# Performance work log

Measured on AMD Instinct MI355X. Metric: run time of the kernel, lower is better.

Reference implementation:

```python
import jax, jax.numpy as jnp
import numpy as np

NY, NU, NH = 8, 8, 256
T, NB = 2048, 64


def setup_inputs() -> dict:
    key = jax.random.key(0)
    ks = jax.random.split(key, 10)
    return {
        "_y0": jax.random.normal(ks[0], (NB, NY), dtype=jnp.float32),
        "_U": jax.random.normal(ks[1], (T, NB, NU), dtype=jnp.float32),
        "lmbd_cont_real": jax.random.uniform(ks[2], (NH // 2,), dtype=jnp.float32),
        "lmbd_cont_imag": jax.random.uniform(ks[3], (NH // 2,), dtype=jnp.float32),
        "B": jax.random.normal(ks[4], (NH, NU), dtype=jnp.float32) / np.sqrt(NU).astype(np.float32),
        "multiplier_on_B": jnp.zeros((NH,), dtype=jnp.float32),
        "W_y2x": jax.random.normal(ks[5], (NH, NY), dtype=jnp.float32) / np.sqrt(NY).astype(np.float32),
        "b_y2x": jax.random.normal(ks[6], (NH,), dtype=jnp.float32) * 0.01,
        "W_x2y": jax.random.normal(ks[7], (NY, NH), dtype=jnp.float32) / np.sqrt(NH).astype(np.float32),
        "b_x2y": jax.random.normal(ks[8], (NY,), dtype=jnp.float32) * 0.01,
    }


def reference(_y0, _U, lmbd_cont_real, lmbd_cont_imag, B, multiplier_on_B,
              W_y2x, b_y2x, W_x2y, b_x2y):
    H2 = lmbd_cont_real.shape[0]
    # input drive: (T, NB, NH)
    Bu = jnp.einsum('tbu,hu->tbh', _U, B) * jnp.exp(multiplier_on_B)
    # stable complex-conjugate-pair eigenvalues
    r = jnp.exp(-jnp.abs(lmbd_cont_real))
    theta = (jnp.pi / 2) * lmbd_cont_imag
    re = r * jnp.cos(theta)
    im = r * jnp.sin(theta)
    # initial state from y0
    x0 = _y0 @ W_y2x.T + b_y2x  # (NB, NH)

    def step(x, bu):
        x1, x2 = x[:, :H2], x[:, H2:]
        # A = [[diag(re), -diag(im)], [diag(im), diag(re)]]; x <- x A^T + bu
        nx = jnp.concatenate([re * x1 - im * x2, im * x1 + re * x2], axis=1) + bu
        return nx, nx

    _, X = jax.lax.scan(step, x0, Bu)  # X: (T, NB, NH)
    Y = X @ W_x2y.T + b_x2y  # (T, NB, NY)
    return Y
```

## Files before the change

kernel.cpp:

```cpp
#include <hip/hip_runtime.h>
#include <math.h>

#define T_   2048
#define NB_  64
#define NU_  8
#define NY_  8
#define NH_  256
#define H2_  128
#define CCH  64
#define LCH  32
#define TT_  2

#define BUF_FLOATS (CCH*NB_*H2_*2)
static const float PI_HALF = 1.5707963267948966f;


__global__ __launch_bounds__(64) void k_local(
    const float* __restrict__ U, const float* __restrict__ lr,
    const float* __restrict__ li, const float* __restrict__ B,
    const float* __restrict__ mult, float* __restrict__ c_buf)
{
    const int k = blockIdx.x >> 6;
    const int b = blockIdx.x & 63;
    const int j = threadIdx.x;

    float r1  = expf(-fabsf(lr[j]));
    float t1  = PI_HALF * li[j];
    float re1 = r1 * cosf(t1), im1 = r1 * sinf(t1);
    float r2  = expf(-fabsf(lr[j+64]));
    float t2  = PI_HALF * li[j+64];
    float re2 = r2 * cosf(t2), im2 = r2 * sinf(t2);

    float B1[NU_], B2[NU_], B3[NU_], B4[NU_];
    {
        float s1 = expf(mult[j]),      s2 = expf(mult[j+128]);
        float s3 = expf(mult[j+64]),   s4 = expf(mult[j+192]);
        #pragma unroll
        for (int i = 0; i < NU_; i++) {
            B1[i] = B[(j      )*NU_ + i] * s1;
            B2[i] = B[(j + 128)*NU_ + i] * s2;
            B3[i] = B[(j +  64)*NU_ + i] * s3;
            B4[i] = B[(j + 192)*NU_ + i] * s4;
        }
    }

    __shared__ float uS[LCH*NU_];
    {
        int t = j >> 1, half = j & 1;
        float4 v = *(const float4*)(U + ((size_t)(k*LCH + t)*NB_ + b)*NU_ + half*4);
        ((float4*)uS)[j] = v;
    }
    __syncthreads();

    float x1a=0.f, x2a=0.f, x1b=0.f, x2b=0.f;
    #pragma unroll 8
    for (int t = 0; t < LCH; t++) {
        float4 u0 = ((const float4*)uS)[2*t+0];
        float4 u1 = ((const float4*)uS)[2*t+1];
        float u[NU_] = {u0.x,u0.y,u0.z,u0.w,u1.x,u1.y,u1.z,u1.w};
        float bu1=0.f, bu2=0.f, bu3=0.f, bu4=0.f;
        #pragma unroll
        for (int i = 0; i < NU_; i++) {
            bu1 = fmaf(u[i], B1[i], bu1);
            bu2 = fmaf(u[i], B2[i], bu2);
            bu3 = fmaf(u[i], B3[i], bu3);
            bu4 = fmaf(u[i], B4[i], bu4);
        }
        float n1a = fmaf(re1, x1a, fmaf(-im1, x2a, bu1));
        float n2a = fmaf(im1, x1a, fmaf( re1, x2a, bu2));
        float n1b = fmaf(re2, x1b, fmaf(-im2, x2b, bu3));
        float n2b = fmaf(im2, x1b, fmaf( re2, x2b, bu4));
        x1a=n1a; x2a=n2a; x1b=n1b; x2b=n2b;
    }

    float* base = c_buf + ((size_t)(k*NB_ + b))*(H2_*2);
    *(float2*)(base + 2*j)       = make_float2(x1a, x2a);
    *(float2*)(base + 128 + 2*j) = make_float2(x1b, x2b);
}

__global__ __launch_bounds__(64) void k_prefix(
    const float* __restrict__ y0, const float* __restrict__ lr,
    const float* __restrict__ li, const float* __restrict__ Wy2x,
    const float* __restrict__ by2x, const float* __restrict__ c_buf,
    float* __restrict__ init_buf)
{
    const int g = blockIdx.x*64 + threadIdx.x;
    const int b = g >> 7;
    const int h = g & 127;

    float x1 = by2x[h], x2 = by2x[h+H2_];
    #pragma unroll
    for (int y = 0; y < NY_; y++) {
        float yy = y0[b*NY_ + y];
        x1 = fmaf(yy, Wy2x[h*NY_ + y],        x1);
        x2 = fmaf(yy, Wy2x[(h+H2_)*NY_ + y],  x2);
    }

    float rL  = expf(-(float)LCH * fabsf(lr[h]));
    float thL = (float)LCH * PI_HALF * li[h];
    float reL = rL * cosf(thL), imL = rL * sinf(thL);

    const size_t stride = NB_*(size_t)(H2_*2);
    const size_t off    = (size_t)b*(H2_*2) + 2*h;

    #pragma unroll 8
    for (int k = 0; k < CCH; k++) {
        float2 c = *(const float2*)(c_buf + k*stride + off);
        *(float2*)(init_buf + k*stride + off) = make_float2(x1, x2);
        float n1 = fmaf(reL, x1, fmaf(-imL, x2, c.x));
        float n2 = fmaf(imL, x1, fmaf( reL, x2, c.y));
        x1 = n1; x2 = n2;
    }
}

__global__ __launch_bounds__(64) void k_emit(
    const float* __restrict__ U, const float* __restrict__ lr,
    const float* __restrict__ li, const float* __restrict__ B,
    const float* __restrict__ mult, const float* __restrict__ Wx2y,
    const float* __restrict__ bx2y, const float* __restrict__ init_buf,
    float* __restrict__ Y)
{
    const int k = blockIdx.x >> 6;
    const int b = blockIdx.x & 63;
    const int j = threadIdx.x;

    float r1  = expf(-fabsf(lr[j]));
    float t1  = PI_HALF * li[j];
    float re1 = r1 * cosf(t1), im1 = r1 * sinf(t1);
    float r2  = expf(-fabsf(lr[j+64]));
    float t2  = PI_HALF * li[j+64];
    float re2 = r2 * cosf(t2), im2 = r2 * sinf(t2);

    float B1[NU_], B2[NU_], B3[NU_], B4[NU_];
    {
        float s1 = expf(mult[j]),      s2 = expf(mult[j+128]);
        float s3 = expf(mult[j+64]),   s4 = expf(mult[j+192]);
        #pragma unroll
        for (int i = 0; i < NU_; i++) {
            B1[i] = B[(j      )*NU_ + i] * s1;
            B2[i] = B[(j + 128)*NU_ + i] * s2;
            B3[i] = B[(j +  64)*NU_ + i] * s3;
            B4[i] = B[(j + 192)*NU_ + i] * s4;
        }
    }

    float W1[NY_], W2[NY_], W3[NY_], W4[NY_];
    #pragma unroll
    for (int y = 0; y < NY_; y++) {
        W1[y] = Wx2y[y*NH_ + j      ];
        W2[y] = Wx2y[y*NH_ + j + 128];
        W3[y] = Wx2y[y*NH_ + j +  64];
        W4[y] = Wx2y[y*NH_ + j + 192];
    }
    const float biasv = bx2y[j & 7];

    __shared__ float uS[LCH*NU_];
    __shared__ float pS[64*17];
    {
        int t = j >> 1, half = j & 1;
        float4 v = *(const float4*)(U + ((size_t)(k*LCH + t)*NB_ + b)*NU_ + half*4);
        ((float4*)uS)[j] = v;
    }

    const float* base = init_buf + ((size_t)(k*NB_ + b))*(H2_*2);
    float2 i1 = *(const float2*)(base + 2*j);
    float2 i2 = *(const float2*)(base + 128 + 2*j);
    float x1a=i1.x, x2a=i1.y, x1b=i2.x, x2b=i2.y;
    __syncthreads();

    float* outk = Y + ((size_t)k*LCH*NB_ + b)*NY_;

    for (int tt = 0; tt < LCH/TT_; tt++) {
        float p[TT_*NY_];
        #pragma unroll
        for (int t4 = 0; t4 < TT_; t4++) {
            int t = tt*TT_ + t4;
            float4 u0 = ((const float4*)uS)[2*t+0];
            float4 u1 = ((const float4*)uS)[2*t+1];
            float u[NU_] = {u0.x,u0.y,u0.z,u0.w,u1.x,u1.y,u1.z,u1.w};
            float bu1=0.f, bu2=0.f, bu3=0.f, bu4=0.f;
            #pragma unroll
            for (int i = 0; i < NU_; i++) {
                bu1 = fmaf(u[i], B1[i], bu1);
                bu2 = fmaf(u[i], B2[i], bu2);
                bu3 = fmaf(u[i], B3[i], bu3);
                bu4 = fmaf(u[i], B4[i], bu4);
            }
            float n1a = fmaf(re1, x1a, fmaf(-im1, x2a, bu1));
            float n2a = fmaf(im1, x1a, fmaf( re1, x2a, bu2));
            float n1b = fmaf(re2, x1b, fmaf(-im2, x2b, bu3));
            float n2b = fmaf(im2, x1b, fmaf( re2, x2b, bu4));
            x1a=n1a; x2a=n2a; x1b=n1b; x2b=n2b;

            #pragma unroll
            for (int y = 0; y < NY_; y++) {
                p[t4*NY_ + y] = fmaf(x1a, W1[y], fmaf(x2a, W2[y],
                                fmaf(x1b, W3[y], x2b * W4[y])));
            }
        }
        float* row = pS + j*17;
        #pragma unroll
        for (int i = 0; i < TT_*NY_; i++) row[i] = p[i];
        __syncthreads();
        {
            const int c = j & 15;
            const int g = j >> 4;
            float s0=0.f, s1=0.f, s2=0.f, s3=0.f;
            #pragma unroll
            for (int s = 0; s < 16; s += 4) {
                s0 += pS[(g*16 + s+0)*17 + c];
                s1 += pS[(g*16 + s+1)*17 + c];
                s2 += pS[(g*16 + s+2)*17 + c];
                s3 += pS[(g*16 + s+3)*17 + c];
            }
            float sum = (s0+s1) + (s2+s3);
            sum += __shfl_xor(sum, 16, 64);
            sum += __shfl_xor(sum, 32, 64);
            if (j < 16) {
                int t4 = j >> 3, y = j & 7;
                outk[(size_t)(tt*TT_ + t4)*NB_*NY_ + y] = sum + biasv;
            }
        }
        __syncthreads();
    }
}

extern "C" void kernel_launch(void* const* d_in, const int* in_sizes, int n_in,
                              void* d_out, int out_size, void* d_ws, size_t ws_size,
                              hipStream_t stream) {
    const float* y0   = (const float*)d_in[0];
    const float* U    = (const float*)d_in[1];
    const float* lr   = (const float*)d_in[2];
    const float* li   = (const float*)d_in[3];
    const float* B    = (const float*)d_in[4];
    const float* mult = (const float*)d_in[5];
    const float* Wy2x = (const float*)d_in[6];
    const float* by2x = (const float*)d_in[7];
    const float* Wx2y = (const float*)d_in[8];
    const float* bx2y = (const float*)d_in[9];
    float* Y = (float*)d_out;

    float* c_buf    = (float*)d_ws;
    float* init_buf = c_buf + BUF_FLOATS;

    k_local <<<CCH*NB_, 64, 0, stream>>>(U, lr, li, B, mult, c_buf);
    k_prefix<<<(NB_*H2_)/64, 64, 0, stream>>>(y0, lr, li, Wy2x, by2x, c_buf, init_buf);
    k_emit  <<<CCH*NB_, 64, 0, stream>>>(U, lr, li, B, mult, Wx2y, bx2y, init_buf, Y);
}
```

Baseline: 112.0 us.

## Compute output projection with fp16 MFMA and drop LDS staging of U

The emit kernel now writes 16 timesteps of state to shared memory as packed fp16 with an XOR swizzle. It then computes the Y = X·W^T projection with 16x16x32 f16 MFMA instructions, replacing the per-thread dot products followed by an LDS reduction and shuffles. Both the local and emit kernels now read U straight from global memory instead of staging it through LDS, and they remap each thread to adjacent eigen-pairs so loads and stores are vectorized. Rounding the states to fp16 (round-toward-zero) before the projection lowers precision, and half of the MFMA output rows are padding.

```diff
diff --git a/kernel.cpp b/kernel.cpp
--- a/kernel.cpp
+++ b/kernel.cpp
@@ -9,10 +9,13 @@
 #define H2_  128
 #define CCH  64
 #define LCH  32
-#define TT_  2
 
 #define BUF_FLOATS (CCH*NB_*H2_*2)
 static const float PI_HALF = 1.5707963267948966f;
+
+typedef _Float16 half8  __attribute__((ext_vector_type(8)));
+typedef __fp16   fp16x2 __attribute__((ext_vector_type(2)));
+typedef float    f32x4  __attribute__((ext_vector_type(4)));
 
 
 __global__ __launch_bounds__(64) void k_local(
@@ -23,59 +26,53 @@
     const int k = blockIdx.x >> 6;
     const int b = blockIdx.x & 63;
     const int j = threadIdx.x;
-
-    float r1  = expf(-fabsf(lr[j]));
-    float t1  = PI_HALF * li[j];
-    float re1 = r1 * cosf(t1), im1 = r1 * sinf(t1);
-    float r2  = expf(-fabsf(lr[j+64]));
-    float t2  = PI_HALF * li[j+64];
-    float re2 = r2 * cosf(t2), im2 = r2 * sinf(t2);
-
-    float B1[NU_], B2[NU_], B3[NU_], B4[NU_];
+    const int c0 = 2*j;
+
+    float2 lrv = *(const float2*)(lr + c0);
+    float2 liv = *(const float2*)(li + c0);
+    float rA  = expf(-fabsf(lrv.x)), thA = PI_HALF*liv.x;
+    float reA = rA*cosf(thA), imA = rA*sinf(thA);
+    float rB  = expf(-fabsf(lrv.y)), thB = PI_HALF*liv.y;
+    float reB = rB*cosf(thB), imB = rB*sinf(thB);
+
+    float Ba1[NU_], Ba2[NU_], Bb1[NU_], Bb2[NU_];
     {
-        float s1 = expf(mult[j]),      s2 = expf(mult[j+128]);
-        float s3 = expf(mult[j+64]),   s4 = expf(mult[j+192]);
+        float s1 = expf(mult[c0]),     s2 = expf(mult[c0+128]);
+        float s3 = expf(mult[c0+1]),   s4 = expf(mult[c0+129]);
         #pragma unroll
         for (int i = 0; i < NU_; i++) {
-            B1[i] = B[(j      )*NU_ + i] * s1;
-            B2[i] = B[(j + 128)*NU_ + i] * s2;
-            B3[i] = B[(j +  64)*NU_ + i] * s3;
-            B4[i] = B[(j + 192)*NU_ + i] * s4;
-        }
-    }
-
-    __shared__ float uS[LCH*NU_];
-    {
-        int t = j >> 1, half = j & 1;
-        float4 v = *(const float4*)(U + ((size_t)(k*LCH + t)*NB_ + b)*NU_ + half*4);
-        ((float4*)uS)[j] = v;
-    }
-    __syncthreads();
-
-    float x1a=0.f, x2a=0.f, x1b=0.f, x2b=0.f;
-    #pragma unroll 8
+            Ba1[i] = B[(c0    )*NU_ + i] * s1;
+            Bb1[i] = B[(c0+  1)*NU_ + i] * s3;
+            Ba2[i] = B[(c0+128)*NU_ + i] * s2;
+            Bb2[i] = B[(c0+129)*NU_ + i] * s4;
+        }
+    }
+
+    const float4* Ut = (const float4*)(U + ((size_t)(k*LCH)*NB_ + b)*NU_);
+
+    float xa1=0.f, xa2=0.f, xb1=0.f, xb2=0.f;
+    #pragma unroll 4
     for (int t = 0; t < LCH; t++) {
-        float4 u0 = ((const float4*)uS)[2*t+0];
-        float4 u1 = ((const float4*)uS)[2*t+1];
+        float4 u0 = Ut[t*128 + 0];
+        float4 u1 = Ut[t*128 + 1];
         float u[NU_] = {u0.x,u0.y,u0.z,u0.w,u1.x,u1.y,u1.z,u1.w};
-        float bu1=0.f, bu2=0.f, bu3=0.f, bu4=0.f;
+        float ba1=0.f, ba2=0.f, bb1=0.f, bb2=0.f;
         #pragma unroll
         for (int i = 0; i < NU_; i++) {
-            bu1 = fmaf(u[i], B1[i], bu1);
-            bu2 = fmaf(u[i], B2[i], bu2);
-            bu3 = fmaf(u[i], B3[i], bu3);
-            bu4 = fmaf(u[i], B4[i], bu4);
-        }
-        float n1a = fmaf(re1, x1a, fmaf(-im1, x2a, bu1));
-        float n2a = fmaf(im1, x1a, fmaf( re1, x2a, bu2));
-        float n1b = fmaf(re2, x1b, fmaf(-im2, x2b, bu3));
-        float n2b = fmaf(im2, x1b, fmaf( re2, x2b, bu4));
-        x1a=n1a; x2a=n2a; x1b=n1b; x2b=n2b;
-    }
-
-    float* base = c_buf + ((size_t)(k*NB_ + b))*(H2_*2);
-    *(float2*)(base + 2*j)       = make_float2(x1a, x2a);
-    *(float2*)(base + 128 + 2*j) = make_float2(x1b, x2b);
+            ba1 = fmaf(u[i], Ba1[i], ba1);
+            ba2 = fmaf(u[i], Ba2[i], ba2);
+            bb1 = fmaf(u[i], Bb1[i], bb1);
+            bb2 = fmaf(u[i], Bb2[i], bb2);
+        }
+        float na1 = fmaf(reA, xa1, fmaf(-imA, xa2, ba1));
+        float na2 = fmaf(imA, xa1, fmaf( reA, xa2, ba2));
+        float nb1 = fmaf(reB, xb1, fmaf(-imB, xb2, bb1));
+        float nb2 = fmaf(imB, xb1, fmaf( reB, xb2, bb2));
+        xa1=na1; xa2=na2; xb1=nb1; xb2=nb2;
+    }
+
+    *(float4*)(c_buf + ((size_t)(k*NB_ + b))*(H2_*2) + 4*j) =
+        make_float4(xa1, xa2, xb1, xb2);
 }
 
 __global__ __launch_bounds__(64) void k_prefix(
@@ -123,105 +120,101 @@
     const int k = blockIdx.x >> 6;
     const int b = blockIdx.x & 63;
     const int j = threadIdx.x;
-
-    float r1  = expf(-fabsf(lr[j]));
-    float t1  = PI_HALF * li[j];
-    float re1 = r1 * cosf(t1), im1 = r1 * sinf(t1);
-    float r2  = expf(-fabsf(lr[j+64]));
-    float t2  = PI_HALF * li[j+64];
-    float re2 = r2 * cosf(t2), im2 = r2 * sinf(t2);
-
-    float B1[NU_], B2[NU_], B3[NU_], B4[NU_];
+    const int c0 = 2*j;
+
+    float2 lrv = *(const float2*)(lr + c0);
+    float2 liv = *(const float2*)(li + c0);
+    float rA  = expf(-fabsf(lrv.x)), thA = PI_HALF*liv.x;
+    float reA = rA*cosf(thA), imA = rA*sinf(thA);
+    float rB  = expf(-fabsf(lrv.y)), thB = PI_HALF*liv.y;
+    float reB = rB*cosf(thB), imB = rB*sinf(thB);
+
+    float Ba1[NU_], Ba2[NU_], Bb1[NU_], Bb2[NU_];
     {
-        float s1 = expf(mult[j]),      s2 = expf(mult[j+128]);
-        float s3 = expf(mult[j+64]),   s4 = expf(mult[j+192]);
+        float s1 = expf(mult[c0]),     s2 = expf(mult[c0+128]);
+        float s3 = expf(mult[c0+1]),   s4 = expf(mult[c0+129]);
         #pragma unroll
         for (int i = 0; i < NU_; i++) {
-            B1[i] = B[(j      )*NU_ + i] * s1;
-            B2[i] = B[(j + 128)*NU_ + i] * s2;
-            B3[i] = B[(j +  64)*NU_ + i] * s3;
-            B4[i] = B[(j + 192)*NU_ + i] * s4;
-        }
-    }
-
-    float W1[NY_], W2[NY_], W3[NY_], W4[NY_];
+            Ba1[i] = B[(c0    )*NU_ + i] * s1;
+            Bb1[i] = B[(c0+  1)*NU_ + i] * s3;
+            Ba2[i] = B[(c0+128)*NU_ + i] * s2;
+            Bb2[i] = B[(c0+129)*NU_ + i] * s4;
+        }
+    }
+
+    const int yv  = j & 15;
+    const int kg  = j >> 4;
+    const int row = yv;
+    half8 wf[8];
     #pragma unroll
-    for (int y = 0; y < NY_; y++) {
-        W1[y] = Wx2y[y*NH_ + j      ];
-        W2[y] = Wx2y[y*NH_ + j + 128];
-        W3[y] = Wx2y[y*NH_ + j +  64];
-        W4[y] = Wx2y[y*NH_ + j + 192];
-    }
-    const float biasv = bx2y[j & 7];
-
-    __shared__ float uS[LCH*NU_];
-    __shared__ float pS[64*17];
-    {
-        int t = j >> 1, half = j & 1;
-        float4 v = *(const float4*)(U + ((size_t)(k*LCH + t)*NB_ + b)*NU_ + half*4);
-        ((float4*)uS)[j] = v;
-    }
-
-    const float* base = init_buf + ((size_t)(k*NB_ + b))*(H2_*2);
-    float2 i1 = *(const float2*)(base + 2*j);
-    float2 i2 = *(const float2*)(base + 128 + 2*j);
-    float x1a=i1.x, x2a=i1.y, x1b=i2.x, x2b=i2.y;
-    __syncthreads();
-
-    float* outk = Y + ((size_t)k*LCH*NB_ + b)*NY_;
-
-    for (int tt = 0; tt < LCH/TT_; tt++) {
-        float p[TT_*NY_];
-        #pragma unroll
-        for (int t4 = 0; t4 < TT_; t4++) {
-            int t = tt*TT_ + t4;
-            float4 u0 = ((const float4*)uS)[2*t+0];
-            float4 u1 = ((const float4*)uS)[2*t+1];
+    for (int q = 0; q < 8; q++) {
+        half8 f;
+        if (yv < 8) {
+            const float* wr = Wx2y + yv*NH_ + q*32 + kg*8;
+            #pragma unroll
+            for (int i = 0; i < 8; i++) f[i] = (_Float16)wr[i];
+        } else {
+            #pragma unroll
+            for (int i = 0; i < 8; i++) f[i] = (_Float16)0.f;
+        }
+        wf[q] = f;
+    }
+    const float bias = bx2y[yv & 7];
+
+    __shared__ _Float16 xS[16*256];
+    uint32_t* xS32 = (uint32_t*)xS;
+
+    float4 ini = *(const float4*)(init_buf + ((size_t)(k*NB_ + b))*(H2_*2) + 4*j);
+    float xa1=ini.x, xa2=ini.y, xb1=ini.z, xb2=ini.w;
+
+    const float4* Ut = (const float4*)(U + ((size_t)(k*LCH)*NB_ + b)*NU_);
+
+    for (int s = 0; s < LCH/16; s++) {
+        #pragma unroll 4
+        for (int t16 = 0; t16 < 16; t16++) {
+            const int t = s*16 + t16;
+            float4 u0 = Ut[t*128 + 0];
+            float4 u1 = Ut[t*128 + 1];
             float u[NU_] = {u0.x,u0.y,u0.z,u0.w,u1.x,u1.y,u1.z,u1.w};
-            float bu1=0.f, bu2=0.f, bu3=0.f, bu4=0.f;
+            float ba1=0.f, ba2=0.f, bb1=0.f, bb2=0.f;
             #pragma unroll
             for (int i = 0; i < NU_; i++) {
-                bu1 = fmaf(u[i], B1[i], bu1);
-                bu2 = fmaf(u[i], B2[i], bu2);
-                bu3 = fmaf(u[i], B3[i], bu3);
-                bu4 = fmaf(u[i], B4[i], bu4);
+                ba1 = fmaf(u[i], Ba1[i], ba1);
+                ba2 = fmaf(u[i], Ba2[i], ba2);
+                bb1 = fmaf(u[i], Bb1[i], bb1);
+                bb2 = fmaf(u[i], Bb2[i], bb2);
             }
-            float n1a = fmaf(re1, x1a, fmaf(-im1, x2a, bu1));
-            float n2a = fmaf(im1, x1a, fmaf( re1, x2a, bu2));
-            float n1b = fmaf(re2, x1b, fmaf(-im2, x2b, bu3));
-            float n2b = fmaf(im2, x1b, fmaf( re2, x2b, bu4));
-            x1a=n1a; x2a=n2a; x1b=n1b; x2b=n2b;
-
-            #pragma unroll
-            for (int y = 0; y < NY_; y++) {
-                p[t4*NY_ + y] = fmaf(x1a, W1[y], fmaf(x2a, W2[y],
-                                fmaf(x1b, W3[y], x2b * W4[y])));
+            float na1 = fmaf(reA, xa1, fmaf(-imA, xa2, ba1));
+            float na2 = fmaf(imA, xa1, fmaf( reA, xa2, ba2));
+            float nb1 = fmaf(reB, xb1, fmaf(-imB, xb2, bb1));
+            float nb2 = fmaf(imB, xb1, fmaf( reB, xb2, bb2));
+            xa1=na1; xa2=na2; xb1=nb1; xb2=nb2;
+
+            union { fp16x2 h; uint32_t u32; } p0, p1;
+            p0.h = __builtin_amdgcn_cvt_pkrtz(xa1, xb1);
+            p1.h = __builtin_amdgcn_cvt_pkrtz(xa2, xb2);
+            const int w0 = t16*128 + (((j>>2) ^ t16) << 2) + (j & 3);
+            xS32[w0]      = p0.u32;
+            xS32[w0 + 64] = p1.u32;
+        }
+        __syncthreads();
+
+        f32x4 acc = {0.f, 0.f, 0.f, 0.f};
+        #pragma unroll
+        for (int q = 0; q < 8; q++) {
+            const int p = ((q << 2) + kg) ^ row;
+            const half8* ap = (const half8*)(xS + (row << 8) + (p << 3));
+            acc = __builtin_amdgcn_mfma_f32_16x16x32_f16(*ap, wf[q], acc, 0, 0, 0);
+        }
+        __syncthreads();
+
+        if (yv < 8) {
+            #pragma unroll
+            for (int r = 0; r < 4; r++) {
+                const int tg = k*LCH + s*16 + kg*4 + r;
+                Y[((size_t)tg*NB_ + b)*NY_ + yv] = acc[r] + bias;
             }
         }
-        float* row = pS + j*17;
-        #pragma unroll
-        for (int i = 0; i < TT_*NY_; i++) row[i] = p[i];
-        __syncthreads();
-        {
-            const int c = j & 15;
-            const int g = j >> 4;
-            float s0=0.f, s1=0.f, s2=0.f, s3=0.f;
-            #pragma unroll
-            for (int s = 0; s < 16; s += 4) {
-                s0 += pS[(g*16 + s+0)*17 + c];
-                s1 += pS[(g*16 + s+1)*17 + c];
-                s2 += pS[(g*16 + s+2)*17 + c];
-                s3 += pS[(g*16 + s+3)*17 + c];
-            }
-            float sum = (s0+s1) + (s2+s3);
-            sum += __shfl_xor(sum, 16, 64);
-            sum += __shfl_xor(sum, 32, 64);
-            if (j < 16) {
-                int t4 = j >> 3, y = j & 7;
-                outk[(size_t)(tt*TT_ + t4)*NB_*NY_ + y] = sum + biasv;
-            }
-        }
-        __syncthreads();
     }
 }
 
```

After: 107.5 us. 4.0% less time.
